# Kernel tuning notes

Measured on AMD Instinct MI355X. Metric: run time of the kernel, lower is better.

The kernel has to match this reference:

```python
import jax, jax.numpy as jnp
import numpy as np
from jax import lax

B, T, F = 32, 1024, 40
H = 256          # lstm_cell_size
V = 29           # vocab_size -> CTC head has V+1 outputs


def setup_inputs():
    key = jax.random.key(0)
    ks = jax.random.split(key, 16)

    def w(k, shape, fan):
        return jax.random.normal(k, shape, jnp.float32) / np.sqrt(fan)

    def lstm_bias():
        # zeros with unit forget bias (Keras default), gate order i,f,c,o
        return jnp.zeros((4 * H,), jnp.float32).at[H:2 * H].set(1.0)

    inp = {
        'x': jax.random.normal(ks[0], (B, T, F), jnp.float32),
        'x_len': jax.random.randint(ks[1], (B,), 1, T + 1, dtype=jnp.int32),
    }
    i = 2
    for name, in_dim in [('ws0', F), ('ws1', H), ('wc0', F), ('wc1', H)]:
        inp[name + '_k'] = w(ks[i], (in_dim, 4 * H), in_dim); i += 1
        inp[name + '_r'] = w(ks[i], (H, 4 * H), H); i += 1
        inp[name + '_b'] = lstm_bias()
    inp['ctc_w'] = w(ks[i], (H, V + 1), H)
    inp['ctc_b'] = jnp.zeros((V + 1,), jnp.float32)
    return inp


def seq_mask(lens, t):
    return jnp.arange(t)[None, :] < lens[:, None]  # [B, t] bool


def lstm(x, mask, Wk, Wr, b):
    """Keras LSTM, return_sequences=True, masked steps carry state/output."""
    h0 = jnp.zeros((x.shape[0], H), x.dtype)
    c0 = jnp.zeros((x.shape[0], H), x.dtype)
    xz = jnp.einsum('btf,fg->btg', x, Wk) + b  # [B,T,4H] precomputed input proj

    def step(carry, inp):
        h, c = carry
        zt, mt = inp  # [B,4H], [B]
        z = zt + h @ Wr
        zi, zf, zg, zo = jnp.split(z, 4, axis=-1)
        i = jax.nn.sigmoid(zi)
        f = jax.nn.sigmoid(zf)
        g = jnp.tanh(zg)
        o = jax.nn.sigmoid(zo)
        c_new = f * c + i * g
        h_new = o * jnp.tanh(c_new)
        m = mt[:, None]
        h = jnp.where(m, h_new, h)
        c = jnp.where(m, c_new, c)
        return (h, c), h

    _, ys = lax.scan(step, (h0, c0), (xz.transpose(1, 0, 2), mask.T))
    return ys.transpose(1, 0, 2)  # [B,T,H]


def maxpool3_same(x):
    # MaxPool1D(pool_size=3, strides=3, padding='same') over time axis
    return lax.reduce_window(x, -np.inf, lax.max, (1, 3, 1), (1, 3, 1), 'SAME')


def transcribe(x, x_len, p0, p1):
    out = jnp.clip(x, -3.0, 3.0)
    out = lstm(out, seq_mask(x_len, out.shape[1]), *p0)   # layer 0
    seq_len = ((x_len + 2) // 3).astype(jnp.int32)         # ceil(len/3)
    out = maxpool3_same(out)
    m = seq_mask(seq_len, out.shape[1])
    out = lstm(out, m, *p1)                                # layer 1 (loop)
    out = lstm(out, m, *p1)                                # layer 1 again (trans_layers[-1])
    return out, seq_len


def reference(x, x_len,
              ws0_k, ws0_r, ws0_b, ws1_k, ws1_r, ws1_b,
              wc0_k, wc0_r, wc0_b, wc1_k, wc1_r, wc1_b,
              ctc_w, ctc_b):
    out_s, len_s = transcribe(x, x_len, (ws0_k, ws0_r, ws0_b), (ws1_k, ws1_r, ws1_b))
    ctc_s = out_s @ ctc_w + ctc_b
    out_c, len_c = transcribe(x, x_len, (wc0_k, wc0_r, wc0_b), (wc1_k, wc1_r, wc1_b))
    ctc_c = out_c @ ctc_w + ctc_b
    close = jnp.all(jnp.abs(ctc_s - ctc_c) < 1e-5, axis=(1, 2))
    return ctc_s, len_s, ctc_c, len_c, close
```

## Files before the change

### kernel.cpp

```cpp
#include <hip/hip_runtime.h>


#define HID 256
#define TT  1024
#define TP  342
#define FF  40

typedef float f32x4 __attribute__((ext_vector_type(4)));

__device__ __forceinline__ float sigf(float x)     { return 1.0f / (1.0f + __expf(-x)); }
__device__ __forceinline__ float tanhfast(float x) { return 1.0f - 2.0f / (__expf(2.0f * x) + 1.0f); }

__device__ __forceinline__ void coh_store_u32(unsigned* p, unsigned v) {
    asm volatile("global_store_dword %0, %1, off sc0 sc1"
                 :: "v"(p), "v"(v) : "memory");
}
__device__ __forceinline__ float untag(float v) {
    return __uint_as_float(__float_as_uint(v) & 0xFFFFFF00u);
}

__device__ __forceinline__ void poll3(const float* p0, const float* p1, const float* p2,
                                      unsigned tag, float& r0, float& r1, float& r2) {
    float x0, x1, x2, y0, y1, y2;
    unsigned t0, t1;
    asm volatile(
        "global_load_dword %[x0], %[p0], off sc0 sc1\n\t"
        "global_load_dword %[x1], %[p1], off sc0 sc1\n\t"
        "global_load_dword %[x2], %[p2], off sc0 sc1\n\t"
        "1:\n\t"
        "global_load_dword %[y0], %[p0], off sc0 sc1\n\t"
        "global_load_dword %[y1], %[p1], off sc0 sc1\n\t"
        "global_load_dword %[y2], %[p2], off sc0 sc1\n\t"
        "s_waitcnt vmcnt(3)\n\t"
        "v_xor_b32 %[t0], %[x0], %[tag]\n\t"
        "v_xor_b32 %[t1], %[x1], %[tag]\n\t"
        "v_or_b32 %[t0], %[t0], %[t1]\n\t"
        "v_xor_b32 %[t1], %[x2], %[tag]\n\t"
        "v_or_b32 %[t0], %[t0], %[t1]\n\t"
        "v_and_b32 %[t0], 0xff, %[t0]\n\t"
        "v_cmp_ne_u32 vcc, 0, %[t0]\n\t"
        "s_cbranch_vccz 2f\n\t"
        "global_load_dword %[x0], %[p0], off sc0 sc1\n\t"
        "global_load_dword %[x1], %[p1], off sc0 sc1\n\t"
        "global_load_dword %[x2], %[p2], off sc0 sc1\n\t"
        "s_waitcnt vmcnt(3)\n\t"
        "v_xor_b32 %[t0], %[y0], %[tag]\n\t"
        "v_xor_b32 %[t1], %[y1], %[tag]\n\t"
        "v_or_b32 %[t0], %[t0], %[t1]\n\t"
        "v_xor_b32 %[t1], %[y2], %[tag]\n\t"
        "v_or_b32 %[t0], %[t0], %[t1]\n\t"
        "v_and_b32 %[t0], 0xff, %[t0]\n\t"
        "v_cmp_ne_u32 vcc, 0, %[t0]\n\t"
        "s_cbranch_vccnz 1b\n\t"
        "s_waitcnt vmcnt(0)\n\t"
        "v_mov_b32 %[x0], %[y0]\n\t"
        "v_mov_b32 %[x1], %[y1]\n\t"
        "v_mov_b32 %[x2], %[y2]\n\t"
        "s_branch 3f\n\t"
        "2:\n\t"
        "s_waitcnt vmcnt(0)\n\t"
        "3:\n\t"
        : [x0]"=&v"(x0), [x1]"=&v"(x1), [x2]"=&v"(x2),
          [y0]"=&v"(y0), [y1]"=&v"(y1), [y2]"=&v"(y2),
          [t0]"=&v"(t0), [t1]"=&v"(t1)
        : [p0]"v"(p0), [p1]"v"(p1), [p2]"v"(p2), [tag]"v"(tag)
        : "vcc", "memory");
    r0 = x0; r1 = x1; r2 = x2;
}

__global__ __launch_bounds__(512, 2) void lstm1_kernel(
    const float* __restrict__ x, const int* __restrict__ x_len,
    const float* __restrict__ Wk_s, const float* __restrict__ Wr_s, const float* __restrict__ b_s,
    const float* __restrict__ Wk_c, const float* __restrict__ Wr_c, const float* __restrict__ b_c,
    float* __restrict__ hbuf,
    float* __restrict__ pooled)
{
    const int blk = blockIdx.x;
    const int q   = blk >> 6;
    const int grp = blk & 63;
    const int br  = grp >> 5;
    const int s   = grp & 31;
    const int tid = threadIdx.x;
    const int u   = tid & 63;
    const int rg  = tid >> 6;
    const int col0 = q * 64 + u;

    const float* Wk = br ? Wk_c : Wk_s;
    const float* Wr = br ? Wr_c : Wr_s;
    const float* bb = br ? b_c  : b_s;

    float w[4][32];
#pragma unroll
    for (int g = 0; g < 4; ++g)
#pragma unroll
        for (int k = 0; k < 32; ++k)
            w[g][k] = Wr[(size_t)(rg * 32 + k) * 1024 + g * 256 + col0];

    float wk[4][8];
    if (rg >= 3) {
#pragma unroll
        for (int g = 0; g < 4; ++g)
#pragma unroll
            for (int j = 0; j < 8; ++j)
                wk[g][j] = Wk[(size_t)((rg - 3) * 8 + j) * 1024 + g * 256 + col0];
    }

    float bias[4] = {0.f, 0.f, 0.f, 0.f};
    if (rg == 0) {
#pragma unroll
        for (int g = 0; g < 4; ++g) bias[g] = bb[g * 256 + col0];
    }

    const int len = x_len[s];
    float cst = 0.f, hcur = 0.f, pm = -1e30f;

    __shared__ float h_lds[256];
    __shared__ float part[8][4][64];

    const int q1 = (q + 1) & 3, q2 = (q + 2) & 3, q3 = (q + 3) & 3;

    for (int t = 0; t < TT; ++t) {
        if (t < len) {
            float acc[4] = {0.f, 0.f, 0.f, 0.f};
            if (rg >= 3) {
                const float* xr = x + ((size_t)s * TT + t) * FF + (rg - 3) * 8;
#pragma unroll
                for (int j = 0; j < 8; ++j) {
                    float v = xr[j];
                    v = fminf(fmaxf(v, -3.f), 3.f);
#pragma unroll
                    for (int g = 0; g < 4; ++g) acc[g] += v * wk[g][j];
                }
            }
            if (rg == 0) {
                const float* hb = hbuf + ((size_t)(t & 1) * 64 + grp) * 256;
                float r0, r1, r2;
                poll3(hb + q1 * 64 + u, hb + q2 * 64 + u, hb + q3 * 64 + u,
                      (unsigned)t & 0xFFu, r0, r1, r2);
                h_lds[q1 * 64 + u] = untag(r0);
                h_lds[q2 * 64 + u] = untag(r1);
                h_lds[q3 * 64 + u] = untag(r2);
                h_lds[q  * 64 + u] = hcur;
            }
            __syncthreads();

            f32x4 hv[8];
            const f32x4* hp = (const f32x4*)&h_lds[rg * 32];
#pragma unroll
            for (int i = 0; i < 8; ++i) hv[i] = hp[i];
#pragma unroll
            for (int i = 0; i < 8; ++i) {
#pragma unroll
                for (int jj = 0; jj < 4; ++jj) {
                    float hh = hv[i][jj];
#pragma unroll
                    for (int g = 0; g < 4; ++g)
                        acc[g] += hh * w[g][i * 4 + jj];
                }
            }
#pragma unroll
            for (int g = 0; g < 4; ++g) part[rg][g][u] = acc[g];
            __syncthreads();

            if (rg == 0) {
                float z[4];
#pragma unroll
                for (int g = 0; g < 4; ++g) {
                    float sum = bias[g];
#pragma unroll
                    for (int r = 0; r < 8; ++r) sum += part[r][g][u];
                    z[g] = sum;
                }
                float ig = sigf(z[0]);
                float fg = sigf(z[1]);
                float gg = tanhfast(z[2]);
                float og = sigf(z[3]);
                cst  = fg * cst + ig * gg;
                hcur = og * tanhfast(cst);
                float* hw = hbuf + ((size_t)((t + 1) & 1) * 64 + grp) * 256;
                unsigned hb32 = (__float_as_uint(hcur) & 0xFFFFFF00u)
                              | ((unsigned)(t + 1) & 0xFFu);
                coh_store_u32((unsigned*)(hw + col0), hb32);
            }
        }
        if (rg == 0) {
            pm = fmaxf(pm, hcur);
            if ((t % 3) == 1) {
                int tp = (t - 1) / 3;
                pooled[(((size_t)br * 32 + s) * TP + tp) * HID + col0] = pm;
                pm = -1e30f;
            }
        }
    }
    if (rg == 0)
        pooled[(((size_t)br * 32 + s) * TP + 341) * HID + col0] = pm;
}

__global__ __launch_bounds__(512, 2) void lstm23_kernel(
    const float* __restrict__ xz,
    const int* __restrict__ x_len,
    const float* __restrict__ Wr_s, const float* __restrict__ Wr_c,
    float* __restrict__ hbuf,
    float* __restrict__ yout)
{
    const int blk = blockIdx.x;
    const int q   = blk >> 6;
    const int grp = blk & 63;
    const int br  = grp >> 5;
    const int s   = grp & 31;
    const int tid = threadIdx.x;
    const int u   = tid & 63;
    const int rg  = tid >> 6;
    const int col0 = q * 64 + u;

    const float* Wr = br ? Wr_c : Wr_s;

    float w[4][32];
#pragma unroll
    for (int g = 0; g < 4; ++g)
#pragma unroll
        for (int k = 0; k < 32; ++k)
            w[g][k] = Wr[(size_t)(rg * 32 + k) * 1024 + g * 256 + col0];

    const int len = (x_len[s] + 2) / 3;
    float cst = 0.f, hcur = 0.f;

    __shared__ float h_lds[256];
    __shared__ float part[8][4][64];

    const int q1 = (q + 1) & 3, q2 = (q + 2) & 3, q3 = (q + 3) & 3;

    for (int t = 0; t < TP; ++t) {
        const size_t row = ((size_t)br * 32 + s) * TP + t;
        if (t < len) {
            float xzv[4] = {0.f, 0.f, 0.f, 0.f};
            if (rg == 0) {
#pragma unroll
                for (int g = 0; g < 4; ++g)
                    xzv[g] = xz[row * 1024 + g * 256 + col0];
                const float* hb = hbuf + ((size_t)(t & 1) * 64 + grp) * 256;
                float r0, r1, r2;
                poll3(hb + q1 * 64 + u, hb + q2 * 64 + u, hb + q3 * 64 + u,
                      (unsigned)t & 0xFFu, r0, r1, r2);
                h_lds[q1 * 64 + u] = untag(r0);
                h_lds[q2 * 64 + u] = untag(r1);
                h_lds[q3 * 64 + u] = untag(r2);
                h_lds[q  * 64 + u] = hcur;
            }
            __syncthreads();

            f32x4 hv[8];
            const f32x4* hp = (const f32x4*)&h_lds[rg * 32];
#pragma unroll
            for (int i = 0; i < 8; ++i) hv[i] = hp[i];
            float acc[4] = {0.f, 0.f, 0.f, 0.f};
#pragma unroll
            for (int i = 0; i < 8; ++i) {
#pragma unroll
                for (int jj = 0; jj < 4; ++jj) {
                    float hh = hv[i][jj];
#pragma unroll
                    for (int g = 0; g < 4; ++g)
                        acc[g] += hh * w[g][i * 4 + jj];
                }
            }
#pragma unroll
            for (int g = 0; g < 4; ++g) part[rg][g][u] = acc[g];
            __syncthreads();

            if (rg == 0) {
                float z[4];
#pragma unroll
                for (int g = 0; g < 4; ++g) {
                    float sum = xzv[g];
#pragma unroll
                    for (int r = 0; r < 8; ++r) sum += part[r][g][u];
                    z[g] = sum;
                }
                float ig = sigf(z[0]);
                float fg = sigf(z[1]);
                float gg = tanhfast(z[2]);
                float og = sigf(z[3]);
                cst  = fg * cst + ig * gg;
                hcur = og * tanhfast(cst);
                float* hw = hbuf + ((size_t)((t + 1) & 1) * 64 + grp) * 256;
                unsigned hb32 = (__float_as_uint(hcur) & 0xFFFFFF00u)
                              | ((unsigned)(t + 1) & 0xFFu);
                coh_store_u32((unsigned*)(hw + col0), hb32);
            }
        }
        if (rg == 0)
            yout[row * HID + col0] = hcur;
    }
}

__global__ __launch_bounds__(256) void gemm_xz(
    const float* __restrict__ A,
    const float* __restrict__ Ws, const float* __restrict__ Wc,
    const float* __restrict__ bs, const float* __restrict__ bc,
    float* __restrict__ out)
{
    __shared__ float As[32][68];
    __shared__ float Bs[32][132];
    const int tid = threadIdx.x;
    const int bx = blockIdx.x, by = blockIdx.y;
    const int row0 = by * 64, col0 = bx * 128;
    const int br = (by >= 171);
    const float* W    = br ? Wc : Ws;
    const float* bias = br ? bc : bs;
    const int tx = tid & 15, ty = tid >> 4;

    float acc[4][8];
#pragma unroll
    for (int i = 0; i < 4; ++i)
#pragma unroll
        for (int j = 0; j < 8; ++j) acc[i][j] = 0.f;

    for (int k0 = 0; k0 < 256; k0 += 32) {
#pragma unroll
        for (int i = 0; i < 2; ++i) {
            int c = tid * 2 + i;
            int r = c >> 3, kv = c & 7;
            float4 v = *(const float4*)(A + (size_t)(row0 + r) * 256 + k0 + kv * 4);
            As[kv * 4 + 0][r] = v.x; As[kv * 4 + 1][r] = v.y;
            As[kv * 4 + 2][r] = v.z; As[kv * 4 + 3][r] = v.w;
        }
#pragma unroll
        for (int i = 0; i < 4; ++i) {
            int c = tid + i * 256;
            int kr = c >> 5, nv = c & 31;
            *(float4*)&Bs[kr][nv * 4] =
                *(const float4*)(W + (size_t)(k0 + kr) * 1024 + col0 + nv * 4);
        }
        __syncthreads();
#pragma unroll
        for (int k = 0; k < 32; ++k) {
            float4 a  = *(const float4*)&As[k][ty * 4];
            float4 b0 = *(const float4*)&Bs[k][tx * 8];
            float4 b1 = *(const float4*)&Bs[k][tx * 8 + 4];
            float av[4] = {a.x, a.y, a.z, a.w};
            float bv[8] = {b0.x, b0.y, b0.z, b0.w, b1.x, b1.y, b1.z, b1.w};
#pragma unroll
            for (int i = 0; i < 4; ++i)
#pragma unroll
                for (int j = 0; j < 8; ++j)
                    acc[i][j] += av[i] * bv[j];
        }
        __syncthreads();
    }
    float bv[8];
#pragma unroll
    for (int j = 0; j < 8; ++j) bv[j] = bias[col0 + tx * 8 + j];
#pragma unroll
    for (int i = 0; i < 4; ++i) {
        int r = row0 + ty * 4 + i;
        float4 o0 = {acc[i][0] + bv[0], acc[i][1] + bv[1], acc[i][2] + bv[2], acc[i][3] + bv[3]};
        float4 o1 = {acc[i][4] + bv[4], acc[i][5] + bv[5], acc[i][6] + bv[6], acc[i][7] + bv[7]};
        float* po = out + (size_t)r * 1024 + col0 + tx * 8;
        *(float4*)(po)     = o0;
        *(float4*)(po + 4) = o1;
    }
}

__global__ __launch_bounds__(256) void ctc_kernel(
    const float* __restrict__ Y,
    const float* __restrict__ Wct,
    const float* __restrict__ bct,
    float* __restrict__ dout)
{
    __shared__ float wl[256 * 30];
    __shared__ float yl[8][257];
    const int tid = threadIdx.x;
    const int row0 = blockIdx.x * 8;

    for (int i = tid; i < 7680; i += 256) wl[i] = Wct[i];
#pragma unroll
    for (int i = 0; i < 8; ++i) {
        int c = tid + i * 256;
        int r = c >> 8, k = c & 255;
        yl[r][k] = Y[(size_t)(row0 + r) * 256 + k];
    }
    __syncthreads();

    const int v = tid & 31, r = tid >> 5;
    if (v < 30) {
        float acc = bct[v];
#pragma unroll 8
        for (int k = 0; k < 256; ++k) acc += yl[r][k] * wl[k * 30 + v];
        int gr = row0 + r;
        int br = gr / 10944;
        int rr = gr - br * 10944;
        dout[(br ? 328352 : 0) + (size_t)rr * 30 + v] = acc;
    }
}

__global__ __launch_bounds__(256) void finalize_kernel(
    const int* __restrict__ x_len, float* __restrict__ dout)
{
    const int b = blockIdx.x, tid = threadIdx.x;
    const float* cs = dout + (size_t)b * 10260;
    const float* cc = dout + 328352 + (size_t)b * 10260;
    __shared__ int flag;
    if (tid == 0) flag = 1;
    __syncthreads();
    bool ok = true;
    for (int i = tid; i < 10260; i += 256)
        ok &= (fabsf(cs[i] - cc[i]) < 1e-5f);
    if (!ok) atomicAnd(&flag, 0);
    __syncthreads();
    if (tid == 0) {
        float L = (float)((x_len[b] + 2) / 3);
        dout[328320 + b] = L;
        dout[656672 + b] = L;
        dout[656704 + b] = flag ? 1.0f : 0.0f;
    }
}

extern "C" void kernel_launch(void* const* d_in, const int* in_sizes, int n_in,
                              void* d_out, int out_size, void* d_ws, size_t ws_size,
                              hipStream_t stream)
{
    (void)in_sizes; (void)n_in; (void)out_size;
    const float* x     = (const float*)d_in[0];
    const int*   x_len = (const int*)  d_in[1];
    const float* ws0_k = (const float*)d_in[2];
    const float* ws0_r = (const float*)d_in[3];
    const float* ws0_b = (const float*)d_in[4];
    const float* ws1_k = (const float*)d_in[5];
    const float* ws1_r = (const float*)d_in[6];
    const float* ws1_b = (const float*)d_in[7];
    const float* wc0_k = (const float*)d_in[8];
    const float* wc0_r = (const float*)d_in[9];
    const float* wc0_b = (const float*)d_in[10];
    const float* wc1_k = (const float*)d_in[11];
    const float* wc1_r = (const float*)d_in[12];
    const float* wc1_b = (const float*)d_in[13];
    const float* ctc_w = (const float*)d_in[14];
    const float* ctc_b = (const float*)d_in[15];
    float* out = (float*)d_out;
    char*  ws  = (char*)d_ws;

    const size_t h_bytes  = 3ull * 2 * 64 * 256 * sizeof(float);
    const size_t off_b0   = h_bytes;
    const size_t b0_bytes = 2ull * 32 * 342 * 256 * sizeof(float);
    const size_t off_b1   = off_b0 + b0_bytes;
    const size_t b1_bytes = 2ull * 32 * 342 * 1024 * sizeof(float);
    if (ws_size < off_b1 + b1_bytes) return;

    float* h1 = (float*)ws;
    float* h2 = h1 + 2 * 64 * 256;
    float* h3 = h2 + 2 * 64 * 256;
    float* buf0 = (float*)(ws + off_b0);
    float* buf1 = (float*)(ws + off_b1);

    hipMemsetAsync(ws, 0, h_bytes, stream);

    lstm1_kernel<<<256, 512, 0, stream>>>(x, x_len, ws0_k, ws0_r, ws0_b,
                                          wc0_k, wc0_r, wc0_b, h1, buf0);
    gemm_xz<<<dim3(8, 342), 256, 0, stream>>>(buf0, ws1_k, wc1_k, ws1_b, wc1_b, buf1);
    lstm23_kernel<<<256, 512, 0, stream>>>(buf1, x_len, ws1_r, wc1_r, h2, buf0);
    gemm_xz<<<dim3(8, 342), 256, 0, stream>>>(buf0, ws1_k, wc1_k, ws1_b, wc1_b, buf1);
    lstm23_kernel<<<256, 512, 0, stream>>>(buf1, x_len, ws1_r, wc1_r, h3, buf0);
    ctc_kernel<<<2736, 256, 0, stream>>>(buf0, ctc_w, ctc_b, out);
    finalize_kernel<<<32, 256, 0, stream>>>(x_len, out);
}
```

Baseline: 2.305 ms.

## Deepen spin-poll pipeline, prefetch next-step inputs, vectorize partial-sum LDS layout

The cross-block polling loop now keeps three rounds of coherent loads in flight instead of two, which shortens the latency to observe a peer's tagged hidden state. Both LSTM kernels prefetch the next timestep's input (x rows or precomputed xz gates) after the current step's work, taking the global load off the serial critical path. The partial-sum LDS buffer is laid out as float4 per lane so the gate reduction uses vector LDS reads. The costs are more VGPRs and extra in-flight memory traffic while polling.

New measurement: 2.145 ms. -7.0%, faster.

```diff
diff --git a/kernel.cpp b/kernel.cpp
--- a/kernel.cpp
+++ b/kernel.cpp
@@ -21,51 +21,73 @@
 
 __device__ __forceinline__ void poll3(const float* p0, const float* p1, const float* p2,
                                       unsigned tag, float& r0, float& r1, float& r2) {
-    float x0, x1, x2, y0, y1, y2;
+    float a0, a1, a2, b0, b1, b2, c0, c1, c2;
     unsigned t0, t1;
     asm volatile(
-        "global_load_dword %[x0], %[p0], off sc0 sc1\n\t"
-        "global_load_dword %[x1], %[p1], off sc0 sc1\n\t"
-        "global_load_dword %[x2], %[p2], off sc0 sc1\n\t"
+        "global_load_dword %[a0], %[p0], off sc0 sc1\n\t"
+        "global_load_dword %[a1], %[p1], off sc0 sc1\n\t"
+        "global_load_dword %[a2], %[p2], off sc0 sc1\n\t"
+        "global_load_dword %[b0], %[p0], off sc0 sc1\n\t"
+        "global_load_dword %[b1], %[p1], off sc0 sc1\n\t"
+        "global_load_dword %[b2], %[p2], off sc0 sc1\n\t"
         "1:\n\t"
-        "global_load_dword %[y0], %[p0], off sc0 sc1\n\t"
-        "global_load_dword %[y1], %[p1], off sc0 sc1\n\t"
-        "global_load_dword %[y2], %[p2], off sc0 sc1\n\t"
-        "s_waitcnt vmcnt(3)\n\t"
-        "v_xor_b32 %[t0], %[x0], %[tag]\n\t"
-        "v_xor_b32 %[t1], %[x1], %[tag]\n\t"
+        "global_load_dword %[c0], %[p0], off sc0 sc1\n\t"
+        "global_load_dword %[c1], %[p1], off sc0 sc1\n\t"
+        "global_load_dword %[c2], %[p2], off sc0 sc1\n\t"
+        "s_waitcnt vmcnt(6)\n\t"
+        "v_xor_b32 %[t0], %[a0], %[tag]\n\t"
+        "v_xor_b32 %[t1], %[a1], %[tag]\n\t"
         "v_or_b32 %[t0], %[t0], %[t1]\n\t"
-        "v_xor_b32 %[t1], %[x2], %[tag]\n\t"
+        "v_xor_b32 %[t1], %[a2], %[tag]\n\t"
         "v_or_b32 %[t0], %[t0], %[t1]\n\t"
         "v_and_b32 %[t0], 0xff, %[t0]\n\t"
         "v_cmp_ne_u32 vcc, 0, %[t0]\n\t"
         "s_cbranch_vccz 2f\n\t"
-        "global_load_dword %[x0], %[p0], off sc0 sc1\n\t"
-        "global_load_dword %[x1], %[p1], off sc0 sc1\n\t"
-        "global_load_dword %[x2], %[p2], off sc0 sc1\n\t"
-        "s_waitcnt vmcnt(3)\n\t"
-        "v_xor_b32 %[t0], %[y0], %[tag]\n\t"
-        "v_xor_b32 %[t1], %[y1], %[tag]\n\t"
+        "global_load_dword %[a0], %[p0], off sc0 sc1\n\t"
+        "global_load_dword %[a1], %[p1], off sc0 sc1\n\t"
+        "global_load_dword %[a2], %[p2], off sc0 sc1\n\t"
+        "s_waitcnt vmcnt(6)\n\t"
+        "v_xor_b32 %[t0], %[b0], %[tag]\n\t"
+        "v_xor_b32 %[t1], %[b1], %[tag]\n\t"
         "v_or_b32 %[t0], %[t0], %[t1]\n\t"
-        "v_xor_b32 %[t1], %[y2], %[tag]\n\t"
+        "v_xor_b32 %[t1], %[b2], %[tag]\n\t"
+        "v_or_b32 %[t0], %[t0], %[t1]\n\t"
+        "v_and_b32 %[t0], 0xff, %[t0]\n\t"
+        "v_cmp_ne_u32 vcc, 0, %[t0]\n\t"
+        "s_cbranch_vccz 3f\n\t"
+        "global_load_dword %[b0], %[p0], off sc0 sc1\n\t"
+        "global_load_dword %[b1], %[p1], off sc0 sc1\n\t"
+        "global_load_dword %[b2], %[p2], off sc0 sc1\n\t"
+        "s_waitcnt vmcnt(6)\n\t"
+        "v_xor_b32 %[t0], %[c0], %[tag]\n\t"
+        "v_xor_b32 %[t1], %[c1], %[tag]\n\t"
+        "v_or_b32 %[t0], %[t0], %[t1]\n\t"
+        "v_xor_b32 %[t1], %[c2], %[tag]\n\t"
         "v_or_b32 %[t0], %[t0], %[t1]\n\t"
         "v_and_b32 %[t0], 0xff, %[t0]\n\t"
         "v_cmp_ne_u32 vcc, 0, %[t0]\n\t"
         "s_cbranch_vccnz 1b\n\t"
         "s_waitcnt vmcnt(0)\n\t"
-        "v_mov_b32 %[x0], %[y0]\n\t"
-        "v_mov_b32 %[x1], %[y1]\n\t"
-        "v_mov_b32 %[x2], %[y2]\n\t"
-        "s_branch 3f\n\t"
+        "v_mov_b32 %[a0], %[c0]\n\t"
+        "v_mov_b32 %[a1], %[c1]\n\t"
+        "v_mov_b32 %[a2], %[c2]\n\t"
+        "s_branch 5f\n\t"
         "2:\n\t"
         "s_waitcnt vmcnt(0)\n\t"
+        "s_branch 5f\n\t"
         "3:\n\t"
-        : [x0]"=&v"(x0), [x1]"=&v"(x1), [x2]"=&v"(x2),
-          [y0]"=&v"(y0), [y1]"=&v"(y1), [y2]"=&v"(y2),
+        "s_waitcnt vmcnt(0)\n\t"
+        "v_mov_b32 %[a0], %[b0]\n\t"
+        "v_mov_b32 %[a1], %[b1]\n\t"
+        "v_mov_b32 %[a2], %[b2]\n\t"
+        "5:\n\t"
+        : [a0]"=&v"(a0), [a1]"=&v"(a1), [a2]"=&v"(a2),
+          [b0]"=&v"(b0), [b1]"=&v"(b1), [b2]"=&v"(b2),
+          [c0]"=&v"(c0), [c1]"=&v"(c1), [c2]"=&v"(c2),
           [t0]"=&v"(t0), [t1]"=&v"(t1)
         : [p0]"v"(p0), [p1]"v"(p1), [p2]"v"(p2), [tag]"v"(tag)
         : "vcc", "memory");
-    r0 = x0; r1 = x1; r2 = x2;
+    r0 = a0; r1 = a1; r2 = a2;
 }
 
 __global__ __launch_bounds__(512, 2) void lstm1_kernel(
@@ -105,7 +127,7 @@
                 wk[g][j] = Wk[(size_t)((rg - 3) * 8 + j) * 1024 + g * 256 + col0];
     }
 
-    float bias[4] = {0.f, 0.f, 0.f, 0.f};
+    f32x4 bias = {0.f, 0.f, 0.f, 0.f};
     if (rg == 0) {
 #pragma unroll
         for (int g = 0; g < 4; ++g) bias[g] = bb[g * 256 + col0];
@@ -115,19 +137,24 @@
     float cst = 0.f, hcur = 0.f, pm = -1e30f;
 
     __shared__ float h_lds[256];
-    __shared__ float part[8][4][64];
+    __shared__ f32x4 part[8][64];
 
     const int q1 = (q + 1) & 3, q2 = (q + 2) & 3, q3 = (q + 3) & 3;
+
+    float xv[8];
+    if (rg >= 3) {
+        const float* xr = x + (size_t)s * TT * FF + (rg - 3) * 8;
+#pragma unroll
+        for (int j = 0; j < 8; ++j) xv[j] = xr[j];
+    }
 
     for (int t = 0; t < TT; ++t) {
         if (t < len) {
             float acc[4] = {0.f, 0.f, 0.f, 0.f};
             if (rg >= 3) {
-                const float* xr = x + ((size_t)s * TT + t) * FF + (rg - 3) * 8;
 #pragma unroll
                 for (int j = 0; j < 8; ++j) {
-                    float v = xr[j];
-                    v = fminf(fmaxf(v, -3.f), 3.f);
+                    float v = fminf(fmaxf(xv[j], -3.f), 3.f);
 #pragma unroll
                     for (int g = 0; g < 4; ++g) acc[g] += v * wk[g][j];
                 }
@@ -158,23 +185,24 @@
                         acc[g] += hh * w[g][i * 4 + jj];
                 }
             }
-#pragma unroll
-            for (int g = 0; g < 4; ++g) part[rg][g][u] = acc[g];
+            f32x4 pv = {acc[0], acc[1], acc[2], acc[3]};
+            part[rg][u] = pv;
+
+            if (rg >= 3 && t + 1 < len) {
+                const float* xr = x + ((size_t)s * TT + t + 1) * FF + (rg - 3) * 8;
+#pragma unroll
+                for (int j = 0; j < 8; ++j) xv[j] = xr[j];
+            }
             __syncthreads();
 
             if (rg == 0) {
-                float z[4];
-#pragma unroll
-                for (int g = 0; g < 4; ++g) {
-                    float sum = bias[g];
-#pragma unroll
-                    for (int r = 0; r < 8; ++r) sum += part[r][g][u];
-                    z[g] = sum;
-                }
-                float ig = sigf(z[0]);
-                float fg = sigf(z[1]);
-                float gg = tanhfast(z[2]);
-                float og = sigf(z[3]);
+                f32x4 zv = bias;
+#pragma unroll
+                for (int r = 0; r < 8; ++r) zv += part[r][u];
+                float ig = sigf(zv[0]);
+                float fg = sigf(zv[1]);
+                float gg = tanhfast(zv[2]);
+                float og = sigf(zv[3]);
                 cst  = fg * cst + ig * gg;
                 hcur = og * tanhfast(cst);
                 float* hw = hbuf + ((size_t)((t + 1) & 1) * 64 + grp) * 256;
@@ -226,18 +254,25 @@
     float cst = 0.f, hcur = 0.f;
 
     __shared__ float h_lds[256];
-    __shared__ float part[8][4][64];
+    __shared__ f32x4 part[8][64];
 
     const int q1 = (q + 1) & 3, q2 = (q + 2) & 3, q3 = (q + 3) & 3;
+    const size_t row0 = ((size_t)br * 32 + s) * TP;
+
+    float xzn[4];
+    if (rg == 0) {
+#pragma unroll
+        for (int g = 0; g < 4; ++g)
+            xzn[g] = xz[row0 * 1024 + g * 256 + col0];
+    }
 
     for (int t = 0; t < TP; ++t) {
-        const size_t row = ((size_t)br * 32 + s) * TP + t;
+        const size_t row = row0 + t;
         if (t < len) {
-            float xzv[4] = {0.f, 0.f, 0.f, 0.f};
+            float xzv[4];
             if (rg == 0) {
 #pragma unroll
-                for (int g = 0; g < 4; ++g)
-                    xzv[g] = xz[row * 1024 + g * 256 + col0];
+                for (int g = 0; g < 4; ++g) xzv[g] = xzn[g];
                 const float* hb = hbuf + ((size_t)(t & 1) * 64 + grp) * 256;
                 float r0, r1, r2;
                 poll3(hb + q1 * 64 + u, hb + q2 * 64 + u, hb + q3 * 64 + u,
@@ -264,29 +299,29 @@
                         acc[g] += hh * w[g][i * 4 + jj];
                 }
             }
-#pragma unroll
-            for (int g = 0; g < 4; ++g) part[rg][g][u] = acc[g];
+            f32x4 pv = {acc[0], acc[1], acc[2], acc[3]};
+            part[rg][u] = pv;
             __syncthreads();
 
             if (rg == 0) {
-                float z[4];
-#pragma unroll
-                for (int g = 0; g < 4; ++g) {
-                    float sum = xzv[g];
-#pragma unroll
-                    for (int r = 0; r < 8; ++r) sum += part[r][g][u];
-                    z[g] = sum;
-                }
-                float ig = sigf(z[0]);
-                float fg = sigf(z[1]);
-                float gg = tanhfast(z[2]);
-                float og = sigf(z[3]);
+                f32x4 zv = {xzv[0], xzv[1], xzv[2], xzv[3]};
+#pragma unroll
+                for (int r = 0; r < 8; ++r) zv += part[r][u];
+                float ig = sigf(zv[0]);
+                float fg = sigf(zv[1]);
+                float gg = tanhfast(zv[2]);
+                float og = sigf(zv[3]);
                 cst  = fg * cst + ig * gg;
                 hcur = og * tanhfast(cst);
                 float* hw = hbuf + ((size_t)((t + 1) & 1) * 64 + grp) * 256;
                 unsigned hb32 = (__float_as_uint(hcur) & 0xFFFFFF00u)
                               | ((unsigned)(t + 1) & 0xFFu);
                 coh_store_u32((unsigned*)(hw + col0), hb32);
+                if (t + 1 < len) {
+#pragma unroll
+                    for (int g = 0; g < 4; ++g)
+                        xzn[g] = xz[(row + 1) * 1024 + g * 256 + col0];
+                }
             }
         }
         if (rg == 0)
```
